# Performance work log

Measured on AMD Instinct MI355X. Metric: run time of the kernel, lower is better.

Reference implementation:

```python
import jax, jax.numpy as jnp
import numpy as np

EPS = 1e-5

def _conv(x, w, b, pad):
    # x: [B,C,H,W], w: [O,I,kh,kw] -> [B,O,H',W']
    y = jax.lax.conv_general_dilated(x, w, (1, 1), pad,
                                     dimension_numbers=('NCHW', 'OIHW', 'NCHW'))
    return y + b[None, :, None, None]

def _bn(x, g, b, m, v):
    # inference-mode BatchNorm2d
    s = g / jnp.sqrt(v + EPS)
    return x * s[None, :, None, None] + (b - m * s)[None, :, None, None]

def setup_inputs():
    key = jax.random.key(0)
    ks = jax.random.split(key, 8)
    N, Cin, Cout, H, W, BS = 2, 64, 256, 512, 512, 32
    GH, GW = H // BS, W // BS
    nB = 256
    x = jax.random.normal(ks[0], (N, Cin, H, W), jnp.float32)
    rng = np.random.default_rng(0)
    flat = rng.choice(N * GH * GW, size=nB, replace=False)  # unique blocks
    idx = np.stack([flat // (GH * GW), (flat // GW) % GH, flat % GW], axis=1).astype(np.int32)
    indices = jnp.asarray(idx)             # [nB, 3] = (batch, block_row, block_col)
    mask = jnp.zeros((N, GH, GW), jnp.bool_).at[indices[:, 0], indices[:, 1], indices[:, 2]].set(True)
    def wgt(k, shape):
        return jax.random.normal(k, shape, jnp.float32) * 0.05
    z, o = jnp.zeros(Cout, jnp.float32), jnp.ones(Cout, jnp.float32)
    params = dict(
        w1=wgt(ks[1], (Cout, Cin, 1, 1)), b1=z, g1=o, be1=z, m1=z, v1=o,
        w2=wgt(ks[2], (Cout, Cout, 3, 3)), b2=z, g2=o, be2=z, m2=z, v2=o,
        w3=wgt(ks[3], (Cout, Cout, 1, 1)), b3=z, g3=o, be3=z, m3=z, v3=o,
        wd=wgt(ks[4], (Cout, Cin, 1, 1)), bd=z,
    )
    return {"x": x, "mask": mask, "indices": indices, **params,
            "block_size": 32, "block_stride": 32, "block_offset": 0}

def reference(x, mask, indices, w1, b1, g1, be1, m1, v1,
              w2, b2, g2, be2, m2, v2, w3, b3, g3, be3, m3, v3,
              wd, bd, block_size, block_stride, block_offset):
    BS = block_size
    N, Cin, H, W = x.shape
    b = indices[:, 0]
    rows = indices[:, 1, None] * block_stride + block_offset + jnp.arange(BS)  # [nB,BS]
    cols = indices[:, 2, None] * block_stride + block_offset + jnp.arange(BS)  # [nB,BS]
    ci = jnp.arange(Cin)
    # SparseGather: [nB, Cin, BS, BS]
    blocks = x[b[:, None, None, None], ci[None, :, None, None],
               rows[:, None, :, None], cols[:, None, None, :]]
    h = jax.nn.relu(_bn(_conv(blocks, w1, b1, 'VALID'), g1, be1, m1, v1))
    dense_y = jax.nn.relu(_bn(_conv(h, w2, b2, 'SAME'), g2, be2, m2, v2))
    # conv3/bn3 in the original are dead code (inplace-relu aliasing): output unused.
    ybase = _conv(x, wd, bd, 'VALID')  # downsample (in_channels != out_channels)
    Cout = ybase.shape[1]
    co = jnp.arange(Cout)
    # SparseScatter (add=False -> overwrite blocks; indices are unique)
    y = ybase.at[b[:, None, None, None], co[None, :, None, None],
                 rows[:, None, :, None], cols[:, None, None, :]].set(dense_y)
    return y
```

## Files before the change

### kernel.cpp

```cpp
#include <hip/hip_runtime.h>

#define HW 262144
#define EPSF 1e-5f

typedef __attribute__((ext_vector_type(8))) short bf16x8;
typedef __attribute__((ext_vector_type(4))) float f32x4;

__device__ __forceinline__ unsigned short f2bf(float f) {
    unsigned u = __builtin_bit_cast(unsigned, f);
    return (unsigned short)((u + 0x7FFFu + ((u >> 16) & 1u)) >> 16);
}

typedef __attribute__((address_space(3))) unsigned lds_u32_t;
typedef __attribute__((address_space(1))) const unsigned glb_u32_t;
__device__ __forceinline__ void dma16(const void* gsrc, void* ldst) {
    __builtin_amdgcn_global_load_lds((glb_u32_t*)gsrc, (lds_u32_t*)ldst, 16, 0, 0);
}

#define W2WS_OFF 0
#define W1WS_OFF 1212416
#define T1WS_OFF 1249280
#define S2WS_OFF 1250304
#define T2WS_OFF 1251328
#define WDWS_OFF 1252352
#define MSKWS_OFF 1289216

__global__ __launch_bounds__(512) void kmask(const int* __restrict__ indices,
                                             int nB, char* __restrict__ ws) {
    unsigned char* mb = (unsigned char*)(ws + MSKWS_OFF);
    const int t = threadIdx.x;
    if (t < 512) mb[t] = 0;
    __syncthreads();
    if (t < nB) {
        int bn = indices[t*3+0], gh = indices[t*3+1], gw = indices[t*3+2];
        if ((unsigned)bn < 2u && (unsigned)gh < 16u && (unsigned)gw < 16u)
            mb[bn*256 + gh*16 + gw] = 1;
    }
}

__global__ __launch_bounds__(256) void kprep(
    const float* __restrict__ w1, const float* __restrict__ b1,
    const float* __restrict__ g1, const float* __restrict__ be1,
    const float* __restrict__ m1, const float* __restrict__ v1,
    const float* __restrict__ w2, const float* __restrict__ b2,
    const float* __restrict__ g2, const float* __restrict__ be2,
    const float* __restrict__ m2, const float* __restrict__ v2,
    const float* __restrict__ wd,
    char* __restrict__ ws)
{
    unsigned short* w2ws = (unsigned short*)(ws + W2WS_OFF);
    unsigned short* w1ws = (unsigned short*)(ws + W1WS_OFF);
    unsigned short* wdws = (unsigned short*)(ws + WDWS_OFF);
    float* t1ws = (float*)(ws + T1WS_OFF);
    float* s2ws = (float*)(ws + S2WS_OFF);
    float* t2ws = (float*)(ws + T2WS_OFF);

    const int bid = blockIdx.x, t = threadIdx.x;
    if (bid < 2304) {
        int e  = bid*256 + t;
        int hc = e & 31;
        int r1 = e >> 5;
        int tap = r1 % 9;
        int r2 = r1 / 9;
        int co = r2 & 63;
        int q  = r2 >> 6;
        int cz = q & 3, ch = q >> 2;
        float v = w2[(size_t)(cz*64+co)*2304 + (size_t)(ch*32+hc)*9 + tap];
        w2ws[((ch*4+cz)*64+co)*296 + tap*32 + hc] = f2bf(v);
    } else if (bid < 2368) {
        int e = (bid-2304)*256 + t;
        int hc = e >> 6, ci = e & 63;
        float s1 = g1[hc] * rsqrtf(v1[hc] + EPSF);
        w1ws[hc*72 + ci] = f2bf(w1[hc*64+ci] * s1);
    } else if (bid < 2432) {
        int e = (bid-2368)*256 + t;
        int co = e >> 6, ci = e & 63;
        wdws[co*72 + ci] = f2bf(wd[co*64 + ci]);
    } else {
        if (t < 256) {
            float s1 = g1[t] * rsqrtf(v1[t] + EPSF);
            t1ws[t] = (b1[t]-m1[t])*s1 + be1[t];
            float s2 = g2[t] * rsqrtf(v2[t] + EPSF);
            s2ws[t] = s2;
            t2ws[t] = (b2[t]-m2[t])*s2 + be2[t];
        }
    }
}

__global__ __launch_bounds__(256, 2) void k1_mfma(
    const float* __restrict__ x,
    const float* __restrict__ bd, const char* __restrict__ ws,
    const int* __restrict__ bstride, const int* __restrict__ boff,
    float* __restrict__ y)
{
    extern __shared__ char smem[];
    unsigned short* xT  = (unsigned short*)smem;
    unsigned short* wdS = (unsigned short*)(smem + 36864);
    float*          bdS = (float*)(smem + 73728);

    const int t = threadIdx.x, lane = t & 63, w = t >> 6;
    const int m = lane & 15, g = lane >> 4;
    const int bid = blockIdx.x;
    const int n   = bid >> 10;
    const int row = (bid >> 1) & 511;
    const int c0  = (bid & 1) * 256;

    #pragma unroll
    for (int i = 0; i < 9; ++i)
        dma16((const char*)ws + WDWS_OFF + (t + i*256)*16,
              (char*)wdS + (t + i*256)*16);
    if (t < 64) dma16((const char*)bd + t*16, (char*)bdS + t*16);

    const size_t xbase = (size_t)n*64*HW + (size_t)row*512 + c0;
    #pragma unroll 4
    for (int jc = 0; jc < 16; ++jc) {
        int ci = w + 4*jc;
        float4 xv = *(const float4*)&x[xbase + (size_t)ci*HW + lane*4];
        xT[(lane*4+0)*72 + ci] = f2bf(xv.x);
        xT[(lane*4+1)*72 + ci] = f2bf(xv.y);
        xT[(lane*4+2)*72 + ci] = f2bf(xv.z);
        xT[(lane*4+3)*72 + ci] = f2bf(xv.w);
    }

    const int stride = bstride[0], off = boff[0];
    const bool safe = (stride == 32) && (off == 0);
    unsigned long long mv = 0;
    if (safe) {
        const unsigned char* mb = (const unsigned char*)(ws + MSKWS_OFF);
        mv = *(const unsigned long long*)&mb[n*256 + (row>>5)*16 + (bid&1)*8];
    }

    __syncthreads();

    bf16x8 bF[2][4];
    #pragma unroll
    for (int pxf = 0; pxf < 4; ++pxf)
        #pragma unroll
        for (int kk = 0; kk < 2; ++kk)
            bF[kk][pxf] = *(const bf16x8*)&xT[(w*64 + pxf*16 + m)*72 + kk*32 + g*8];

    const size_t ybase = (size_t)(n*256)*HW + (size_t)row*512 + c0;
    #pragma unroll 1
    for (int cof = 0; cof < 16; ++cof) {
        bf16x8 a0 = *(const bf16x8*)&wdS[(cof*16+m)*72 +      g*8];
        bf16x8 a1 = *(const bf16x8*)&wdS[(cof*16+m)*72 + 32 + g*8];
        f32x4 ac[4];
        #pragma unroll
        for (int pxf = 0; pxf < 4; ++pxf) {
            ac[pxf] = (f32x4){0.f,0.f,0.f,0.f};
            ac[pxf] = __builtin_amdgcn_mfma_f32_16x16x32_bf16(a0, bF[0][pxf], ac[pxf], 0, 0, 0);
            ac[pxf] = __builtin_amdgcn_mfma_f32_16x16x32_bf16(a1, bF[1][pxf], ac[pxf], 0, 0, 0);
        }
        #pragma unroll
        for (int pxf = 0; pxf < 4; ++pxf) {
            const int pxg = w*4 + pxf;
            const bool skip = safe && (((mv >> ((pxg>>1)*8)) & 0xffull) != 0ull);
            if (!skip) {
                #pragma unroll
                for (int j = 0; j < 4; ++j) {
                    const int co = cof*16 + g*4 + j;
                    y[ybase + (size_t)co*HW + pxg*16 + m] = ac[pxf][j] + bdS[co];
                }
            }
        }
    }
}

#define DMA_CZH(CH, CZH)                                                      \
    {                                                                         \
        const char* s_ = (const char*)w2ws                                    \
                         + (size_t)(CH)*151552 + (size_t)(CZH)*75776;         \
        _Pragma("unroll")                                                     \
        for (int i_ = 0; i_ < 9; ++i_)                                        \
            dma16(s_ + t*16 + i_*8192, (char*)w2S + t*16 + i_*8192);          \
        if (t < 128) dma16(s_ + 73728 + t*16, (char*)w2S + 73728 + t*16);     \
    }

#define CONV2_CZH(CZH)                                                        \
    {                                                                         \
        __builtin_amdgcn_s_setprio(1);                                        \
        _Pragma("unroll")                                                     \
        for (int tap = 0; tap < 9; ++tap) {                                   \
            const int dy = tap/3, dx = tap%3;                                 \
            bf16x8 aF[4];                                                     \
            _Pragma("unroll")                                                 \
            for (int cof = 0; cof < 4; ++cof)                                 \
                aF[cof] = *(const bf16x8*)&w2S[(cog*64 + cof*16 + m)*296      \
                                               + tap*32 + g*8];               \
            _Pragma("unroll")                                                 \
            for (int pxf = 0; pxf < 4; ++pxf) {                               \
                int p_ = (ph*2 + (pxf>>1) + dy)*34 + (pxf&1)*16 + m + dx;     \
                bf16x8 bFr = *(const bf16x8*)&hS[p_*40 + g*8];                \
                _Pragma("unroll")                                             \
                for (int cof = 0; cof < 4; ++cof)                             \
                    acc[CZH][cof][pxf] = __builtin_amdgcn_mfma_f32_16x16x32_bf16( \
                        aF[cof], bFr, acc[CZH][cof][pxf], 0, 0, 0);           \
            }                                                                 \
        }                                                                     \
        __builtin_amdgcn_s_setprio(0);                                        \
    }

__global__ __launch_bounds__(512, 2) void k2_fused(
    const float* __restrict__ x, const int* __restrict__ indices,
    const char* __restrict__ ws,
    const int* __restrict__ bstride, const int* __restrict__ boff,
    float* __restrict__ y)
{
    extern __shared__ char smem[];
    unsigned short* xT  = (unsigned short*)smem;
    unsigned short* w1s = (unsigned short*)(smem + 50688);
    unsigned short* hS  = (unsigned short*)(smem + 55296);
    unsigned short* w2S = (unsigned short*)(smem + 83456);
    float* t1S = (float*)(smem + 159232);
    float* s2S = (float*)(smem + 160256);
    float* t2S = (float*)(smem + 161280);

    const unsigned short* w2ws = (const unsigned short*)(ws + W2WS_OFF);
    const unsigned short* w1ws = (const unsigned short*)(ws + W1WS_OFF);

    const int t    = threadIdx.x;
    const int lane = t & 63;
    const int w    = t >> 6;
    const int m    = lane & 15;
    const int g    = lane >> 4;
    const int cog  = w >> 2;
    const int ph   = w & 3;

    const int bid = blockIdx.x;
    const int blk = bid >> 2, pz = bid & 3;
    const int bn = indices[blk*3+0], gr = indices[blk*3+1], gc = indices[blk*3+2];
    const int stride = bstride[0], off = boff[0];
    const int row0 = gr*stride + off, col0 = gc*stride + off;

    if (t < 192) {
        const float* src = (t < 64) ? (const float*)(ws + T1WS_OFF)
                         : (t < 128) ? (const float*)(ws + S2WS_OFF)
                                     : (const float*)(ws + T2WS_OFF);
        float* dst = (t < 64) ? t1S : (t < 128) ? s2S : t2S;
        dma16(src + (lane)*4, dst + (lane)*4);
    }

    {
        const int half = lane >> 5, cc = lane & 31;
        for (int pb = w*80; pb < w*80 + 80; pb += 2) {
            int pi = pb + half;
            int r = pi >> 6, ci = pi & 63;
            int br = pz*8 + r - 1;
            if ((unsigned)br < 32u) {
                float xv = x[(size_t)bn*64*HW + (size_t)ci*HW
                             + (size_t)(row0+br)*512 + (col0+cc)];
                xT[(r*34 + cc + 1)*72 + ci] = f2bf(xv);
            }
        }
    }

    f32x4 acc[2][4][4];
    #pragma unroll
    for (int a = 0; a < 2; ++a)
        #pragma unroll
        for (int b = 0; b < 4; ++b)
            #pragma unroll
            for (int c = 0; c < 4; ++c) acc[a][b][c] = (f32x4){0.f,0.f,0.f,0.f};

    #pragma unroll 1
    for (int ch = 0; ch < 8; ++ch) {
        __syncthreads();

        if (t < 288) dma16((const char*)w1ws + ch*4608 + t*16, (char*)w1s + t*16);
        DMA_CZH(ch, 0);
        __syncthreads();

        f32x4 a1[3][2];
        #pragma unroll
        for (int i = 0; i < 3; ++i) { a1[i][0] = (f32x4){0,0,0,0}; a1[i][1] = (f32x4){0,0,0,0}; }
        #pragma unroll
        for (int i = 0; i < 3; ++i) {
            const int tile = w*3 + i;
            if (tile < 22) {
                #pragma unroll
                for (int kk = 0; kk < 2; ++kk) {
                    bf16x8 bF = *(const bf16x8*)&xT[(tile*16 + m)*72 + kk*32 + g*8];
                    #pragma unroll
                    for (int hct = 0; hct < 2; ++hct) {
                        bf16x8 aF = *(const bf16x8*)&w1s[(hct*16 + m)*72 + kk*32 + g*8];
                        a1[i][hct] = __builtin_amdgcn_mfma_f32_16x16x32_bf16(
                                         aF, bF, a1[i][hct], 0, 0, 0);
                    }
                }
            }
        }
        #pragma unroll
        for (int i = 0; i < 3; ++i) {
            const int tile = w*3 + i;
            if (tile < 22) {
                int p = tile*16 + m;
                int r = p / 34;
                int c = p - r*34;
                int br = pz*8 + r - 1;
                bool valid = (c >= 1) && (c <= 32) && ((unsigned)br < 32u);
                #pragma unroll
                for (int hct = 0; hct < 2; ++hct) {
                    unsigned short hv[4];
                    #pragma unroll
                    for (int j = 0; j < 4; ++j) {
                        float tv = t1S[ch*32 + hct*16 + g*4 + j];
                        float hf = fmaxf(a1[i][hct][j] + tv, 0.f);
                        hv[j] = valid ? f2bf(hf) : (unsigned short)0;
                    }
                    unsigned lo = (unsigned)hv[0] | ((unsigned)hv[1] << 16);
                    unsigned hi = (unsigned)hv[2] | ((unsigned)hv[3] << 16);
                    *(uint2*)&hS[p*40 + hct*16 + g*4] = make_uint2(lo, hi);
                }
            }
        }
        __syncthreads();

        CONV2_CZH(0);
        __syncthreads();
        DMA_CZH(ch, 1);
        __syncthreads();
        CONV2_CZH(1);
    }

    const size_t yblk = (size_t)bn*256*HW;
    const int rbase = row0 + pz*8 + ph*2;
    #pragma unroll
    for (int czh = 0; czh < 2; ++czh) {
        #pragma unroll
        for (int cof = 0; cof < 4; ++cof) {
            #pragma unroll
            for (int j = 0; j < 4; ++j) {
                const int co = czh*128 + cog*64 + cof*16 + g*4 + j;
                float s2 = s2S[co], t2 = t2S[co];
                #pragma unroll
                for (int pxf = 0; pxf < 4; ++pxf) {
                    const int rr = rbase + (pxf>>1);
                    const int cc2 = col0 + (pxf&1)*16 + m;
                    y[yblk + (size_t)co*HW + (size_t)rr*512 + cc2] =
                        fmaxf(fmaf(acc[czh][cof][pxf][j], s2, t2), 0.f);
                }
            }
        }
    }
}

extern "C" void kernel_launch(void* const* d_in, const int* in_sizes, int n_in,
                              void* d_out, int out_size, void* d_ws, size_t ws_size,
                              hipStream_t stream) {
    const float* x       = (const float*)d_in[0];
    const int*   indices = (const int*)  d_in[2];
    const float* w1  = (const float*)d_in[3];
    const float* b1  = (const float*)d_in[4];
    const float* g1  = (const float*)d_in[5];
    const float* be1 = (const float*)d_in[6];
    const float* m1  = (const float*)d_in[7];
    const float* v1  = (const float*)d_in[8];
    const float* w2  = (const float*)d_in[9];
    const float* b2  = (const float*)d_in[10];
    const float* g2  = (const float*)d_in[11];
    const float* be2 = (const float*)d_in[12];
    const float* m2  = (const float*)d_in[13];
    const float* v2  = (const float*)d_in[14];
    const float* wd  = (const float*)d_in[21];
    const float* bd  = (const float*)d_in[22];
    const int* bstride = (const int*)d_in[24];
    const int* boff    = (const int*)d_in[25];
    float* y = (float*)d_out;
    char* ws = (char*)d_ws;

    const int nB = in_sizes[2] / 3;

    hipLaunchKernelGGL(kmask, dim3(1), dim3(512), 0, stream, indices, nB, ws);
    hipLaunchKernelGGL(kprep, dim3(2433), dim3(256), 0, stream,
                       w1, b1, g1, be1, m1, v1, w2, b2, g2, be2, m2, v2, wd, ws);
    hipLaunchKernelGGL(k1_mfma, dim3(2048), dim3(256), 74752, stream,
                       x, bd, ws, bstride, boff, y);
    hipLaunchKernelGGL(k2_fused, dim3(nB * 4), dim3(512), 162304, stream,
                       x, indices, ws, bstride, boff, y);
}
```

Baseline: 462.7 us.

## Pipeline conv1 of next chunk with conv2 and reuse h fragments across taps

The conv1 for the next channel chunk is computed while the conv2 weight DMA for the current chunk is in flight. Its activation and BN write into LDS is deferred until after the current chunk's conv2, and the w1 weights are prefetched two chunks ahead. The conv2 inner loop is reordered by dx so that each loaded h fragment serves three dy taps, which cuts LDS reads of the activation tile. In exchange, keeping a1 and three sets of weight fragments live raises register pressure, which risks spills under the 512x2 launch bound.

```diff
diff --git a/kernel.cpp b/kernel.cpp
--- a/kernel.cpp
+++ b/kernel.cpp
@@ -143,13 +143,13 @@
     #pragma unroll 1
     for (int cof = 0; cof < 16; ++cof) {
         bf16x8 a0 = *(const bf16x8*)&wdS[(cof*16+m)*72 +      g*8];
-        bf16x8 a1 = *(const bf16x8*)&wdS[(cof*16+m)*72 + 32 + g*8];
+        bf16x8 a1w = *(const bf16x8*)&wdS[(cof*16+m)*72 + 32 + g*8];
         f32x4 ac[4];
         #pragma unroll
         for (int pxf = 0; pxf < 4; ++pxf) {
             ac[pxf] = (f32x4){0.f,0.f,0.f,0.f};
-            ac[pxf] = __builtin_amdgcn_mfma_f32_16x16x32_bf16(a0, bF[0][pxf], ac[pxf], 0, 0, 0);
-            ac[pxf] = __builtin_amdgcn_mfma_f32_16x16x32_bf16(a1, bF[1][pxf], ac[pxf], 0, 0, 0);
+            ac[pxf] = __builtin_amdgcn_mfma_f32_16x16x32_bf16(a0,  bF[0][pxf], ac[pxf], 0, 0, 0);
+            ac[pxf] = __builtin_amdgcn_mfma_f32_16x16x32_bf16(a1w, bF[1][pxf], ac[pxf], 0, 0, 0);
         }
         #pragma unroll
         for (int pxf = 0; pxf < 4; ++pxf) {
@@ -176,25 +176,83 @@
         if (t < 128) dma16(s_ + 73728 + t*16, (char*)w2S + 73728 + t*16);     \
     }
 
+#define CONV1_TO_A1()                                                         \
+    {                                                                         \
+        _Pragma("unroll")                                                     \
+        for (int i = 0; i < 3; ++i) {                                         \
+            a1[i][0] = (f32x4){0.f,0.f,0.f,0.f};                              \
+            a1[i][1] = (f32x4){0.f,0.f,0.f,0.f};                              \
+            const int tile = w*3 + i;                                         \
+            if (tile < 22) {                                                  \
+                _Pragma("unroll")                                             \
+                for (int kk = 0; kk < 2; ++kk) {                              \
+                    bf16x8 bF1 = *(const bf16x8*)&xT[(tile*16+m)*72 + kk*32 + g*8]; \
+                    _Pragma("unroll")                                         \
+                    for (int hct = 0; hct < 2; ++hct) {                       \
+                        bf16x8 aF1 = *(const bf16x8*)&w1s[(hct*16+m)*72 + kk*32 + g*8]; \
+                        a1[i][hct] = __builtin_amdgcn_mfma_f32_16x16x32_bf16( \
+                                         aF1, bF1, a1[i][hct], 0, 0, 0);      \
+                    }                                                         \
+                }                                                             \
+            }                                                                 \
+        }                                                                     \
+    }
+
+#define HWRITE(CHX)                                                           \
+    {                                                                         \
+        _Pragma("unroll")                                                     \
+        for (int i = 0; i < 3; ++i) {                                         \
+            const int tile = w*3 + i;                                         \
+            if (tile < 22) {                                                  \
+                int p = tile*16 + m;                                          \
+                int r = p / 34, c = p - r*34;                                 \
+                int br = pz*8 + r - 1;                                        \
+                bool valid = (c >= 1) && (c <= 32) && ((unsigned)br < 32u);   \
+                _Pragma("unroll")                                             \
+                for (int hct = 0; hct < 2; ++hct) {                           \
+                    unsigned short hv[4];                                     \
+                    _Pragma("unroll")                                         \
+                    for (int j = 0; j < 4; ++j) {                             \
+                        float tv = t1S[(CHX)*32 + hct*16 + g*4 + j];          \
+                        float hf = fmaxf(a1[i][hct][j] + tv, 0.f);            \
+                        hv[j] = valid ? f2bf(hf) : (unsigned short)0;         \
+                    }                                                         \
+                    unsigned lo = (unsigned)hv[0] | ((unsigned)hv[1] << 16);  \
+                    unsigned hi = (unsigned)hv[2] | ((unsigned)hv[3] << 16);  \
+                    *(uint2*)&hS[p*40 + hct*16 + g*4] = make_uint2(lo, hi);   \
+                }                                                             \
+            }                                                                 \
+        }                                                                     \
+    }
+
 #define CONV2_CZH(CZH)                                                        \
     {                                                                         \
         __builtin_amdgcn_s_setprio(1);                                        \
         _Pragma("unroll")                                                     \
-        for (int tap = 0; tap < 9; ++tap) {                                   \
-            const int dy = tap/3, dx = tap%3;                                 \
-            bf16x8 aF[4];                                                     \
+        for (int dx = 0; dx < 3; ++dx) {                                      \
+            bf16x8 aF[3][4];                                                  \
             _Pragma("unroll")                                                 \
-            for (int cof = 0; cof < 4; ++cof)                                 \
-                aF[cof] = *(const bf16x8*)&w2S[(cog*64 + cof*16 + m)*296      \
-                                               + tap*32 + g*8];               \
-            _Pragma("unroll")                                                 \
-            for (int pxf = 0; pxf < 4; ++pxf) {                               \
-                int p_ = (ph*2 + (pxf>>1) + dy)*34 + (pxf&1)*16 + m + dx;     \
-                bf16x8 bFr = *(const bf16x8*)&hS[p_*40 + g*8];                \
+            for (int dy = 0; dy < 3; ++dy)                                    \
                 _Pragma("unroll")                                             \
                 for (int cof = 0; cof < 4; ++cof)                             \
-                    acc[CZH][cof][pxf] = __builtin_amdgcn_mfma_f32_16x16x32_bf16( \
-                        aF[cof], bFr, acc[CZH][cof][pxf], 0, 0, 0);           \
+                    aF[dy][cof] = *(const bf16x8*)&w2S[(cog*64 + cof*16 + m)*296 \
+                                                       + (dy*3+dx)*32 + g*8]; \
+            _Pragma("unroll")                                                 \
+            for (int chf = 0; chf < 2; ++chf) {                               \
+                bf16x8 bFr[4];                                                \
+                _Pragma("unroll")                                             \
+                for (int ro = 0; ro < 4; ++ro)                                \
+                    bFr[ro] = *(const bf16x8*)&hS[((ph*2+ro)*34 + chf*16 + m + dx)*40 + g*8]; \
+                _Pragma("unroll")                                             \
+                for (int dy = 0; dy < 3; ++dy)                                \
+                    _Pragma("unroll")                                         \
+                    for (int pr = 0; pr < 2; ++pr)                            \
+                        _Pragma("unroll")                                     \
+                        for (int cof = 0; cof < 4; ++cof)                     \
+                            acc[CZH][cof][pr*2+chf] =                         \
+                                __builtin_amdgcn_mfma_f32_16x16x32_bf16(      \
+                                    aF[dy][cof], bFr[pr+dy],                  \
+                                    acc[CZH][cof][pr*2+chf], 0, 0, 0);        \
             }                                                                 \
         }                                                                     \
         __builtin_amdgcn_s_setprio(0);                                        \
@@ -239,6 +297,7 @@
         float* dst = (t < 64) ? t1S : (t < 128) ? s2S : t2S;
         dma16(src + (lane)*4, dst + (lane)*4);
     }
+    if (t < 288) dma16((const char*)w1ws + t*16, (char*)w1s + t*16);
 
     {
         const int half = lane >> 5, cc = lane & 31;
@@ -262,64 +321,31 @@
             #pragma unroll
             for (int c = 0; c < 4; ++c) acc[a][b][c] = (f32x4){0.f,0.f,0.f,0.f};
 
+    f32x4 a1[3][2];
+
+    __syncthreads();
+    CONV1_TO_A1();
+    __syncthreads();
+    if (t < 288) dma16((const char*)w1ws + 4608 + t*16, (char*)w1s + t*16);
+    HWRITE(0);
+    __syncthreads();
+
     #pragma unroll 1
     for (int ch = 0; ch < 8; ++ch) {
+        DMA_CZH(ch, 0);
+        if (ch < 7) { CONV1_TO_A1(); }
         __syncthreads();
-
-        if (t < 288) dma16((const char*)w1ws + ch*4608 + t*16, (char*)w1s + t*16);
-        DMA_CZH(ch, 0);
-        __syncthreads();
-
-        f32x4 a1[3][2];
-        #pragma unroll
-        for (int i = 0; i < 3; ++i) { a1[i][0] = (f32x4){0,0,0,0}; a1[i][1] = (f32x4){0,0,0,0}; }
-        #pragma unroll
-        for (int i = 0; i < 3; ++i) {
-            const int tile = w*3 + i;
-            if (tile < 22) {
-                #pragma unroll
-                for (int kk = 0; kk < 2; ++kk) {
-                    bf16x8 bF = *(const bf16x8*)&xT[(tile*16 + m)*72 + kk*32 + g*8];
-                    #pragma unroll
-                    for (int hct = 0; hct < 2; ++hct) {
-                        bf16x8 aF = *(const bf16x8*)&w1s[(hct*16 + m)*72 + kk*32 + g*8];
-                        a1[i][hct] = __builtin_amdgcn_mfma_f32_16x16x32_bf16(
-                                         aF, bF, a1[i][hct], 0, 0, 0);
-                    }
-                }
-            }
-        }
-        #pragma unroll
-        for (int i = 0; i < 3; ++i) {
-            const int tile = w*3 + i;
-            if (tile < 22) {
-                int p = tile*16 + m;
-                int r = p / 34;
-                int c = p - r*34;
-                int br = pz*8 + r - 1;
-                bool valid = (c >= 1) && (c <= 32) && ((unsigned)br < 32u);
-                #pragma unroll
-                for (int hct = 0; hct < 2; ++hct) {
-                    unsigned short hv[4];
-                    #pragma unroll
-                    for (int j = 0; j < 4; ++j) {
-                        float tv = t1S[ch*32 + hct*16 + g*4 + j];
-                        float hf = fmaxf(a1[i][hct][j] + tv, 0.f);
-                        hv[j] = valid ? f2bf(hf) : (unsigned short)0;
-                    }
-                    unsigned lo = (unsigned)hv[0] | ((unsigned)hv[1] << 16);
-                    unsigned hi = (unsigned)hv[2] | ((unsigned)hv[3] << 16);
-                    *(uint2*)&hS[p*40 + hct*16 + g*4] = make_uint2(lo, hi);
-                }
-            }
-        }
-        __syncthreads();
-
         CONV2_CZH(0);
         __syncthreads();
         DMA_CZH(ch, 1);
+        if (ch < 6) {
+            if (t < 288) dma16((const char*)w1ws + (ch+2)*4608 + t*16,
+                               (char*)w1s + t*16);
+        }
         __syncthreads();
         CONV2_CZH(1);
+        __syncthreads();
+        if (ch < 7) { HWRITE(ch+1); }
     }
 
     const size_t yblk = (size_t)bn*256*HW;
```

After: 498.6 us. 7.7% more time.

## Split conv2 output channels across blocks and read w2 fragments directly from global

Applied to the files above, without the earlier changes.

The fused sparse-block kernel now splits the 256 output channels into two halves across separate workgroups, doubling the grid. conv2 weights are prepacked in MFMA fragment order and loaded straight from global/L2 instead of being DMA'd into LDS. This cuts shared memory per block enough to allow higher occupancy (launch bounds 4). The hS fragments are reused across dy taps, and the w1 chunk for the next step is prefetched during conv2. The trade-off is that conv1 (h) is recomputed twice per block, and conv2 now depends on global-load latency for weights rather than LDS.

```diff
diff --git a/kernel.cpp b/kernel.cpp
--- a/kernel.cpp
+++ b/kernel.cpp
@@ -57,16 +57,17 @@
 
     const int bid = blockIdx.x, t = threadIdx.x;
     if (bid < 2304) {
-        int e  = bid*256 + t;
-        int hc = e & 31;
-        int r1 = e >> 5;
-        int tap = r1 % 9;
-        int r2 = r1 / 9;
-        int co = r2 & 63;
-        int q  = r2 >> 6;
-        int cz = q & 3, ch = q >> 2;
-        float v = w2[(size_t)(cz*64+co)*2304 + (size_t)(ch*32+hc)*9 + tap];
-        w2ws[((ch*4+cz)*64+co)*296 + tap*32 + hc] = f2bf(v);
+        int e_lin = bid*256 + t;
+        int e  = e_lin & 7;
+        int co = (e_lin >> 3) & 127;
+        int g  = (e_lin >> 10) & 3;
+        int r  = e_lin >> 12;
+        int tap = r % 9;
+        int q  = r / 9;
+        int coh = q & 1, ch = q >> 1;
+        int hc = ch*32 + g*8 + e;
+        int co_g = coh*128 + co;
+        w2ws[e_lin] = f2bf(w2[(size_t)co_g*2304 + (size_t)hc*9 + tap]);
     } else if (bid < 2368) {
         int e = (bid-2304)*256 + t;
         int hc = e >> 6, ci = e & 63;
@@ -142,14 +143,14 @@
     const size_t ybase = (size_t)(n*256)*HW + (size_t)row*512 + c0;
     #pragma unroll 1
     for (int cof = 0; cof < 16; ++cof) {
-        bf16x8 a0 = *(const bf16x8*)&wdS[(cof*16+m)*72 +      g*8];
-        bf16x8 a1 = *(const bf16x8*)&wdS[(cof*16+m)*72 + 32 + g*8];
+        bf16x8 a0  = *(const bf16x8*)&wdS[(cof*16+m)*72 +      g*8];
+        bf16x8 a1w = *(const bf16x8*)&wdS[(cof*16+m)*72 + 32 + g*8];
         f32x4 ac[4];
         #pragma unroll
         for (int pxf = 0; pxf < 4; ++pxf) {
             ac[pxf] = (f32x4){0.f,0.f,0.f,0.f};
-            ac[pxf] = __builtin_amdgcn_mfma_f32_16x16x32_bf16(a0, bF[0][pxf], ac[pxf], 0, 0, 0);
-            ac[pxf] = __builtin_amdgcn_mfma_f32_16x16x32_bf16(a1, bF[1][pxf], ac[pxf], 0, 0, 0);
+            ac[pxf] = __builtin_amdgcn_mfma_f32_16x16x32_bf16(a0,  bF[0][pxf], ac[pxf], 0, 0, 0);
+            ac[pxf] = __builtin_amdgcn_mfma_f32_16x16x32_bf16(a1w, bF[1][pxf], ac[pxf], 0, 0, 0);
         }
         #pragma unroll
         for (int pxf = 0; pxf < 4; ++pxf) {
@@ -166,41 +167,7 @@
     }
 }
 
-#define DMA_CZH(CH, CZH)                                                      \
-    {                                                                         \
-        const char* s_ = (const char*)w2ws                                    \
-                         + (size_t)(CH)*151552 + (size_t)(CZH)*75776;         \
-        _Pragma("unroll")                                                     \
-        for (int i_ = 0; i_ < 9; ++i_)                                        \
-            dma16(s_ + t*16 + i_*8192, (char*)w2S + t*16 + i_*8192);          \
-        if (t < 128) dma16(s_ + 73728 + t*16, (char*)w2S + 73728 + t*16);     \
-    }
-
-#define CONV2_CZH(CZH)                                                        \
-    {                                                                         \
-        __builtin_amdgcn_s_setprio(1);                                        \
-        _Pragma("unroll")                                                     \
-        for (int tap = 0; tap < 9; ++tap) {                                   \
-            const int dy = tap/3, dx = tap%3;                                 \
-            bf16x8 aF[4];                                                     \
-            _Pragma("unroll")                                                 \
-            for (int cof = 0; cof < 4; ++cof)                                 \
-                aF[cof] = *(const bf16x8*)&w2S[(cog*64 + cof*16 + m)*296      \
-                                               + tap*32 + g*8];               \
-            _Pragma("unroll")                                                 \
-            for (int pxf = 0; pxf < 4; ++pxf) {                               \
-                int p_ = (ph*2 + (pxf>>1) + dy)*34 + (pxf&1)*16 + m + dx;     \
-                bf16x8 bFr = *(const bf16x8*)&hS[p_*40 + g*8];                \
-                _Pragma("unroll")                                             \
-                for (int cof = 0; cof < 4; ++cof)                             \
-                    acc[CZH][cof][pxf] = __builtin_amdgcn_mfma_f32_16x16x32_bf16( \
-                        aF[cof], bFr, acc[CZH][cof][pxf], 0, 0, 0);           \
-            }                                                                 \
-        }                                                                     \
-        __builtin_amdgcn_s_setprio(0);                                        \
-    }
-
-__global__ __launch_bounds__(512, 2) void k2_fused(
+__global__ __launch_bounds__(512, 4) void k2_fused(
     const float* __restrict__ x, const int* __restrict__ indices,
     const char* __restrict__ ws,
     const int* __restrict__ bstride, const int* __restrict__ boff,
@@ -208,15 +175,14 @@
 {
     extern __shared__ char smem[];
     unsigned short* xT  = (unsigned short*)smem;
-    unsigned short* w1s = (unsigned short*)(smem + 50688);
-    unsigned short* hS  = (unsigned short*)(smem + 55296);
-    unsigned short* w2S = (unsigned short*)(smem + 83456);
-    float* t1S = (float*)(smem + 159232);
-    float* s2S = (float*)(smem + 160256);
-    float* t2S = (float*)(smem + 161280);
-
-    const unsigned short* w2ws = (const unsigned short*)(ws + W2WS_OFF);
+    unsigned short* w1s = (unsigned short*)(smem + 48960);
+    unsigned short* hS  = (unsigned short*)(smem + 53568);
+
+    const unsigned short* w2g  = (const unsigned short*)(ws + W2WS_OFF);
     const unsigned short* w1ws = (const unsigned short*)(ws + W1WS_OFF);
+    const float* t1g = (const float*)(ws + T1WS_OFF);
+    const float* s2g = (const float*)(ws + S2WS_OFF);
+    const float* t2g = (const float*)(ws + T2WS_OFF);
 
     const int t    = threadIdx.x;
     const int lane = t & 63;
@@ -227,19 +193,14 @@
     const int ph   = w & 3;
 
     const int bid = blockIdx.x;
-    const int blk = bid >> 2, pz = bid & 3;
+    const int blk = bid >> 3, pz = (bid >> 1) & 3, coh = bid & 1;
     const int bn = indices[blk*3+0], gr = indices[blk*3+1], gc = indices[blk*3+2];
     const int stride = bstride[0], off = boff[0];
     const int row0 = gr*stride + off, col0 = gc*stride + off;
 
-    if (t < 192) {
-        const float* src = (t < 64) ? (const float*)(ws + T1WS_OFF)
-                         : (t < 128) ? (const float*)(ws + S2WS_OFF)
-                                     : (const float*)(ws + T2WS_OFF);
-        float* dst = (t < 64) ? t1S : (t < 128) ? s2S : t2S;
-        dma16(src + (lane)*4, dst + (lane)*4);
-    }
-
+    const int alo = g*1024 + (cog*64 + m)*8;
+
+    if (t < 288) dma16((const char*)w1ws + t*16, (char*)w1s + t*16);
     {
         const int half = lane >> 5, cc = lane & 31;
         for (int pb = w*80; pb < w*80 + 80; pb += 2) {
@@ -254,37 +215,33 @@
         }
     }
 
-    f32x4 acc[2][4][4];
+    f32x4 acc[4][4];
     #pragma unroll
-    for (int a = 0; a < 2; ++a)
-        #pragma unroll
-        for (int b = 0; b < 4; ++b)
-            #pragma unroll
-            for (int c = 0; c < 4; ++c) acc[a][b][c] = (f32x4){0.f,0.f,0.f,0.f};
+    for (int a = 0; a < 4; ++a)
+        #pragma unroll
+        for (int b = 0; b < 4; ++b) acc[a][b] = (f32x4){0.f,0.f,0.f,0.f};
+
+    __syncthreads();
 
     #pragma unroll 1
     for (int ch = 0; ch < 8; ++ch) {
-        __syncthreads();
-
-        if (t < 288) dma16((const char*)w1ws + ch*4608 + t*16, (char*)w1s + t*16);
-        DMA_CZH(ch, 0);
-        __syncthreads();
-
+        float4 t1v0 = *(const float4*)&t1g[ch*32      + g*4];
+        float4 t1v1 = *(const float4*)&t1g[ch*32 + 16 + g*4];
         f32x4 a1[3][2];
         #pragma unroll
-        for (int i = 0; i < 3; ++i) { a1[i][0] = (f32x4){0,0,0,0}; a1[i][1] = (f32x4){0,0,0,0}; }
-        #pragma unroll
         for (int i = 0; i < 3; ++i) {
+            a1[i][0] = (f32x4){0.f,0.f,0.f,0.f};
+            a1[i][1] = (f32x4){0.f,0.f,0.f,0.f};
             const int tile = w*3 + i;
             if (tile < 22) {
                 #pragma unroll
                 for (int kk = 0; kk < 2; ++kk) {
-                    bf16x8 bF = *(const bf16x8*)&xT[(tile*16 + m)*72 + kk*32 + g*8];
+                    bf16x8 bF1 = *(const bf16x8*)&xT[(tile*16+m)*72 + kk*32 + g*8];
                     #pragma unroll
                     for (int hct = 0; hct < 2; ++hct) {
-                        bf16x8 aF = *(const bf16x8*)&w1s[(hct*16 + m)*72 + kk*32 + g*8];
+                        bf16x8 aF1 = *(const bf16x8*)&w1s[(hct*16+m)*72 + kk*32 + g*8];
                         a1[i][hct] = __builtin_amdgcn_mfma_f32_16x16x32_bf16(
-                                         aF, bF, a1[i][hct], 0, 0, 0);
+                                         aF1, bF1, a1[i][hct], 0, 0, 0);
                     }
                 }
             }
@@ -294,51 +251,83 @@
             const int tile = w*3 + i;
             if (tile < 22) {
                 int p = tile*16 + m;
-                int r = p / 34;
-                int c = p - r*34;
-                int br = pz*8 + r - 1;
-                bool valid = (c >= 1) && (c <= 32) && ((unsigned)br < 32u);
-                #pragma unroll
-                for (int hct = 0; hct < 2; ++hct) {
-                    unsigned short hv[4];
+                if (p < 340) {
+                    int r = p / 34, c = p - r*34;
+                    int br = pz*8 + r - 1;
+                    bool valid = (c >= 1) && (c <= 32) && ((unsigned)br < 32u);
                     #pragma unroll
-                    for (int j = 0; j < 4; ++j) {
-                        float tv = t1S[ch*32 + hct*16 + g*4 + j];
-                        float hf = fmaxf(a1[i][hct][j] + tv, 0.f);
-                        hv[j] = valid ? f2bf(hf) : (unsigned short)0;
+                    for (int hct = 0; hct < 2; ++hct) {
+                        const float4 tv4 = hct ? t1v1 : t1v0;
+                        unsigned short hv[4];
+                        #pragma unroll
+                        for (int j = 0; j < 4; ++j) {
+                            float hf = fmaxf(a1[i][hct][j] +
+                                             ((const float*)&tv4)[j], 0.f);
+                            hv[j] = valid ? f2bf(hf) : (unsigned short)0;
+                        }
+                        unsigned lo = (unsigned)hv[0] | ((unsigned)hv[1] << 16);
+                        unsigned hi = (unsigned)hv[2] | ((unsigned)hv[3] << 16);
+                        *(uint2*)&hS[p*40 + hct*16 + g*4] = make_uint2(lo, hi);
                     }
-                    unsigned lo = (unsigned)hv[0] | ((unsigned)hv[1] << 16);
-                    unsigned hi = (unsigned)hv[2] | ((unsigned)hv[3] << 16);
-                    *(uint2*)&hS[p*40 + hct*16 + g*4] = make_uint2(lo, hi);
                 }
             }
         }
         __syncthreads();
 
-        CONV2_CZH(0);
+        if (ch < 7 && t < 288)
+            dma16((const char*)w1ws + (ch+1)*4608 + t*16, (char*)w1s + t*16);
+
+        __builtin_amdgcn_s_setprio(1);
+        #pragma unroll
+        for (int dx = 0; dx < 3; ++dx) {
+            bf16x8 bFr[2][4];
+            #pragma unroll
+            for (int chf = 0; chf < 2; ++chf)
+                #pragma unroll
+                for (int ro = 0; ro < 4; ++ro)
+                    bFr[chf][ro] = *(const bf16x8*)
+                        &hS[((ph*2+ro)*34 + chf*16 + m + dx)*40 + g*8];
+            #pragma unroll
+            for (int dy = 0; dy < 3; ++dy) {
+                const int abase = ((ch*2 + coh)*9 + dy*3 + dx) * 4096;
+                bf16x8 aF[4];
+                #pragma unroll
+                for (int cof = 0; cof < 4; ++cof)
+                    aF[cof] = *(const bf16x8*)&w2g[abase + alo + cof*128];
+                #pragma unroll
+                for (int chf = 0; chf < 2; ++chf)
+                    #pragma unroll
+                    for (int pr = 0; pr < 2; ++pr)
+                        #pragma unroll
+                        for (int cof = 0; cof < 4; ++cof)
+                            acc[cof][pr*2+chf] =
+                                __builtin_amdgcn_mfma_f32_16x16x32_bf16(
+                                    aF[cof], bFr[chf][pr+dy],
+                                    acc[cof][pr*2+chf], 0, 0, 0);
+            }
+        }
+        __builtin_amdgcn_s_setprio(0);
         __syncthreads();
-        DMA_CZH(ch, 1);
-        __syncthreads();
-        CONV2_CZH(1);
     }
 
     const size_t yblk = (size_t)bn*256*HW;
     const int rbase = row0 + pz*8 + ph*2;
     #pragma unroll
-    for (int czh = 0; czh < 2; ++czh) {
-        #pragma unroll
-        for (int cof = 0; cof < 4; ++cof) {
+    for (int cof = 0; cof < 4; ++cof) {
+        const int co4 = coh*128 + cog*64 + cof*16 + g*4;
+        float4 s2v = *(const float4*)&s2g[co4];
+        float4 t2v = *(const float4*)&t2g[co4];
+        #pragma unroll
+        for (int j = 0; j < 4; ++j) {
+            const int co = co4 + j;
+            const float s2 = ((const float*)&s2v)[j];
+            const float t2 = ((const float*)&t2v)[j];
             #pragma unroll
-            for (int j = 0; j < 4; ++j) {
-                const int co = czh*128 + cog*64 + cof*16 + g*4 + j;
-                float s2 = s2S[co], t2 = t2S[co];
-                #pragma unroll
-                for (int pxf = 0; pxf < 4; ++pxf) {
-                    const int rr = rbase + (pxf>>1);
-                    const int cc2 = col0 + (pxf&1)*16 + m;
-                    y[yblk + (size_t)co*HW + (size_t)rr*512 + cc2] =
-                        fmaxf(fmaf(acc[czh][cof][pxf][j], s2, t2), 0.f);
-                }
+            for (int pxf = 0; pxf < 4; ++pxf) {
+                const int rr = rbase + (pxf>>1);
+                const int cc2 = col0 + (pxf&1)*16 + m;
+                y[yblk + (size_t)co*HW + (size_t)rr*512 + cc2] =
+                    fmaxf(fmaf(acc[cof][pxf][j], s2, t2), 0.f);
             }
         }
     }
@@ -375,6 +364,6 @@
                        w1, b1, g1, be1, m1, v1, w2, b2, g2, be2, m2, v2, wd, ws);
     hipLaunchKernelGGL(k1_mfma, dim3(2048), dim3(256), 74752, stream,
                        x, bd, ws, bstride, boff, y);
-    hipLaunchKernelGGL(k2_fused, dim3(nB * 4), dim3(512), 162304, stream,
+    hipLaunchKernelGGL(k2_fused, dim3(nB * 8), dim3(512), 80768, stream,
                        x, indices, ws, bstride, boff, y);
 }
```

New measurement: 640.6 us. 1.38x slower.
